# Optimization experiments

Measured on AMD Instinct MI355X. Metric: run time of the kernel, lower is better.

## Reference

```python
import jax, jax.numpy as jnp
import numpy as np

H = 50  # hidden_layer_size

def lstm_layer(x_seq, W_ih, W_hh, b_ih, b_hh):
    """x_seq: [B,T,D]. Returns hidden sequence [T,B,H]. PyTorch gate order i,f,g,o."""
    B = x_seq.shape[0]
    # Precompute input contribution for all timesteps in one GEMM: [B,T,4H]
    xW = jnp.einsum('btd,gd->btg', x_seq, W_ih) + b_ih + b_hh
    xW = jnp.transpose(xW, (1, 0, 2))  # [T,B,4H] for scan over time
    h0 = jnp.zeros((B, H), dtype=x_seq.dtype)
    c0 = jnp.zeros((B, H), dtype=x_seq.dtype)

    def step(carry, xt):
        h, c = carry
        gates = xt + h @ W_hh.T  # [B,4H]
        i, f, g, o = jnp.split(gates, 4, axis=-1)
        i = jax.nn.sigmoid(i)
        f = jax.nn.sigmoid(f)
        g = jnp.tanh(g)
        o = jax.nn.sigmoid(o)
        c = f * c + i * g
        h = o * jnp.tanh(c)
        return (h, c), h

    (_, _), hs = jax.lax.scan(step, (h0, c0), xW)
    return hs  # [T,B,H]


def setup_inputs() -> dict:
    key = jax.random.key(0)
    ks = jax.random.split(key, 12)
    B, T, D = 4096, 512, 5
    s_in = 1.0 / np.sqrt(H)

    def u(k, shape):
        return jax.random.uniform(k, shape, jnp.float32, -s_in, s_in)

    return {
        'input_seq': jax.random.normal(ks[0], (B, T, D), jnp.float32),
        'W_ih_l0': u(ks[1], (4 * H, D)),
        'W_hh_l0': u(ks[2], (4 * H, H)),
        'b_ih_l0': u(ks[3], (4 * H,)),
        'b_hh_l0': u(ks[4], (4 * H,)),
        'W_ih_l1': u(ks[5], (4 * H, H)),
        'W_hh_l1': u(ks[6], (4 * H, H)),
        'b_ih_l1': u(ks[7], (4 * H,)),
        'b_hh_l1': u(ks[8], (4 * H,)),
        'W_lin': u(ks[9], (1, H)),
        'b_lin': u(ks[10], (1,)),
    }


def reference(input_seq, W_ih_l0, W_hh_l0, b_ih_l0, b_hh_l0,
              W_ih_l1, W_hh_l1, b_ih_l1, b_hh_l1, W_lin, b_lin):
    hs0 = lstm_layer(input_seq, W_ih_l0, W_hh_l0, b_ih_l0, b_hh_l0)       # [T,B,H]
    hs1 = lstm_layer(jnp.transpose(hs0, (1, 0, 2)), W_ih_l1, W_hh_l1, b_ih_l1, b_hh_l1)
    last = hs1[-1]                       # [B,H] == out[:, -1, :]
    return last @ W_lin.T + b_lin        # [B,1]
```

## Files before the change

kernel.cpp:

```cpp
#include <hip/hip_runtime.h>

#define TSTEPS 512
#define NB     16
#define NW     13
#define WGS    (NW * 64)

typedef _Float16 f16x8 __attribute__((ext_vector_type(8)));
typedef float    f32x4 __attribute__((ext_vector_type(4)));

#define NKF  4
#define PARF 2048


__global__ __launch_bounds__(WGS)
void lstm_mfma5(const float* __restrict__ x,
                const float* __restrict__ Wih0, const float* __restrict__ Whh0,
                const float* __restrict__ bih0, const float* __restrict__ bhh0,
                const float* __restrict__ Wih1, const float* __restrict__ Whh1,
                const float* __restrict__ bih1, const float* __restrict__ bhh1,
                const float* __restrict__ Wlin, const float* __restrict__ blin,
                float* __restrict__ out)
{
    __shared__ __align__(16) _Float16 Bbuf[2][NKF][64][8];
    __shared__ float h1f[NB][52];

    const int tid    = threadIdx.x;
    const int w      = tid >> 6;
    const int l      = tid & 63;
    const int sg     = l >> 4;
    const int bcol   = l & 15;
    const int batch0 = blockIdx.x * NB;

    _Float16* bbase = &Bbuf[0][0][0][0];

    {
        int* bz = (int*)bbase;
        for (int i = tid; i < 2048; i += WGS) bz[i] = 0;
    }
    __syncthreads();

    auto baddr = [&](int k, int col) -> int {
        int kf = k >> 5, kl = k & 31;
        return (kf * 64 + col + (((kl >> 2) & 3) << 4)) * 8
               + ((kl & 3) | (((kl >> 4) & 1) << 2));
    };

    const bool xact = (tid < NB * 5);
    const int  xb = tid / 5, xd = tid % 5;
    const float* xptr = x + (size_t)(batch0 + xb) * TSTEPS * 5 + xd;
    int xadr = 0;
    if (xact) {
        xadr = baddr(50 + xd, xb);
        bbase[PARF + xadr] = (_Float16)xptr[0];
        bbase[xadr]        = (_Float16)xptr[5];
    }

    f16x8 A0[2], A1[NKF];
    f32x4 bia0, bia1;
    float c0 = 0.f, c1 = 0.f;
    {
        const int arow = w * 16 + bcol;
        const int jj   = arow >> 2;
        const int gt   = arow & 3;
        const bool real = (jj < 50);
        const int row  = gt * 50 + jj;
        const float s  = (gt == 2) ? 2.885390082f : -1.442695041f;
        #pragma unroll
        for (int kf = 0; kf < 2; ++kf) {
            f16x8 a;
            #pragma unroll
            for (int e = 0; e < 8; ++e) {
                int k = kf * 32 + 4 * sg + (e & 3) + ((e >> 2) << 4);
                float v = 0.f;
                if (real) {
                    if (k < 50)      v = Whh0[row * 50 + k];
                    else if (k < 55) v = Wih0[row * 5 + (k - 50)];
                }
                a[e] = (_Float16)(s * v);
            }
            A0[kf] = a;
        }
        #pragma unroll
        for (int kf = 0; kf < NKF; ++kf) {
            f16x8 a;
            #pragma unroll
            for (int e = 0; e < 8; ++e) {
                int k = kf * 32 + 4 * sg + (e & 3) + ((e >> 2) << 4);
                float v = 0.f;
                if (real) {
                    if (k < 50)                  v = Wih1[row * 50 + k];
                    else if (k >= 56 && k < 106) v = Whh1[row * 50 + (k - 56)];
                }
                a[e] = (_Float16)(s * v);
            }
            A1[kf] = a;
        }
    }
    const int j   = 4 * w + sg;
    const bool jok = (j < 50);
    {
        f32x4 b0, b1;
        #pragma unroll
        for (int r = 0; r < 4; ++r) {
            const float sr = (r == 2) ? 2.885390082f : -1.442695041f;
            b0[r] = jok ? sr * (bih0[r * 50 + j] + bhh0[r * 50 + j]) : 0.f;
            b1[r] = jok ? sr * (bih1[r * 50 + j] + bhh1[r * 50 + j]) : 0.f;
        }
        bia0 = b0; bia1 = b1;
    }

    const int adrH0 = jok ? baddr(j, bcol) : 0;
    const int adrH1 = jok ? baddr(56 + j, bcol) : 0;

    auto update = [&](const f32x4& acc, float& c, int wadr) -> float {
        float iv = __builtin_amdgcn_rcpf(1.0f + __builtin_amdgcn_exp2f(acc[0]));
        float fv = __builtin_amdgcn_rcpf(1.0f + __builtin_amdgcn_exp2f(acc[1]));
        float gv = 1.0f - 2.0f * __builtin_amdgcn_rcpf(1.0f + __builtin_amdgcn_exp2f(acc[2]));
        float ov = __builtin_amdgcn_rcpf(1.0f + __builtin_amdgcn_exp2f(acc[3]));
        c = fv * c + iv * gv;
        float th = 1.0f - 2.0f * __builtin_amdgcn_rcpf(1.0f + __builtin_amdgcn_exp2f(2.885390082f * c));
        float h = ov * th;
        if (jok) bbase[wadr] = (_Float16)h;
        return h;
    };

    const _Float16* vbase = &Bbuf[0][0][l][0];
    __syncthreads();

    {
        const _Float16* rd = vbase + PARF;
        f32x4 a = bia0;
        a = __builtin_amdgcn_mfma_f32_16x16x32_f16(A0[0], *(const f16x8*)(rd), a, 0, 0, 0);
        a = __builtin_amdgcn_mfma_f32_16x16x32_f16(A0[1], *(const f16x8*)(rd + 512), a, 0, 0, 0);
        update(a, c0, adrH0);
    }
    float xv_next = xact ? xptr[10] : 0.f;
    __syncthreads();

#define REGION(PAR, T)                                                           \
    {                                                                            \
        const _Float16* rd = vbase + (PAR) * PARF;                               \
        const int wo = ((PAR) ^ 1) * PARF;                                       \
        f16x8 bf0 = *(const f16x8*)(rd);                                         \
        f16x8 bf1 = *(const f16x8*)(rd + 512);                                   \
        f16x8 bf2 = *(const f16x8*)(rd + 1024);                                  \
        f16x8 bf3 = *(const f16x8*)(rd + 1536);                                  \
        if (xact && (T) + 2 < TSTEPS) bbase[wo + xadr] = (_Float16)xv_next;      \
        float xv2 = (xact && (T) + 3 < TSTEPS) ? xptr[((T) + 3) * 5] : 0.f;      \
        f32x4 aB = bia1;                                                         \
        aB = __builtin_amdgcn_mfma_f32_16x16x32_f16(A1[0], bf0, aB, 0, 0, 0);    \
        aB = __builtin_amdgcn_mfma_f32_16x16x32_f16(A1[1], bf1, aB, 0, 0, 0);    \
        aB = __builtin_amdgcn_mfma_f32_16x16x32_f16(A1[2], bf2, aB, 0, 0, 0);    \
        aB = __builtin_amdgcn_mfma_f32_16x16x32_f16(A1[3], bf3, aB, 0, 0, 0);    \
        f32x4 aA = bia0;                                                         \
        aA = __builtin_amdgcn_mfma_f32_16x16x32_f16(A0[0], bf0, aA, 0, 0, 0);    \
        aA = __builtin_amdgcn_mfma_f32_16x16x32_f16(A0[1], bf1, aA, 0, 0, 0);    \
        float h1v = update(aB, c1, wo + adrH1);                                  \
        update(aA, c0, wo + adrH0);                                              \
        if ((T) == TSTEPS - 1 && jok) h1f[bcol][j] = h1v;                        \
        xv_next = xv2;                                                           \
        __syncthreads();                                                         \
    }

    for (int t = 0; t < TSTEPS; t += 2) {
        REGION(0, t)
        REGION(1, t + 1)
    }
#undef REGION

    if (tid < NB) {
        float acc = blin[0];
        #pragma unroll 10
        for (int jj = 0; jj < 50; ++jj) acc += Wlin[jj] * h1f[tid][jj];
        out[batch0 + tid] = acc;
    }
}

extern "C" void kernel_launch(void* const* d_in, const int* in_sizes, int n_in,
                              void* d_out, int out_size, void* d_ws, size_t ws_size,
                              hipStream_t stream) {
    (void)in_sizes; (void)n_in; (void)d_ws; (void)ws_size; (void)out_size;
    const float* x    = (const float*)d_in[0];
    const float* Wih0 = (const float*)d_in[1];
    const float* Whh0 = (const float*)d_in[2];
    const float* bih0 = (const float*)d_in[3];
    const float* bhh0 = (const float*)d_in[4];
    const float* Wih1 = (const float*)d_in[5];
    const float* Whh1 = (const float*)d_in[6];
    const float* bih1 = (const float*)d_in[7];
    const float* bhh1 = (const float*)d_in[8];
    const float* Wlin = (const float*)d_in[9];
    const float* blin = (const float*)d_in[10];
    float* out = (float*)d_out;

    dim3 grid(4096 / NB);
    dim3 block(WGS);
    hipLaunchKernelGGL(lstm_mfma5, grid, block, 0, stream,
                       x, Wih0, Whh0, bih0, bhh0,
                       Wih1, Whh1, bih1, bhh1, Wlin, blin, out);
}
```

Baseline: 354.3 us.

## Fold biases into MFMA via constant-one row, split layer-1 accumulation chain

Places a constant 1.0 in the unused K slot 55 of the shared B operand and stores the combined biases in the matching A-matrix column, so every MFMA chain starts from zero instead of from a bias register. The layer-1 four-MFMA dependent chain is split into two independent two-MFMA chains that are summed afterwards, shortening the serial latency on the recurrent critical path. The per-step __syncthreads is replaced by an explicit lgkmcnt wait, s_barrier and sched_barrier to control scheduling. The trade-offs are an extra vector add per step and the bias now being rounded to fp16.

```diff
diff --git a/kernel.cpp b/kernel.cpp
--- a/kernel.cpp
+++ b/kernel.cpp
@@ -13,7 +13,7 @@
 
 
 __global__ __launch_bounds__(WGS)
-void lstm_mfma5(const float* __restrict__ x,
+void lstm_mfma6(const float* __restrict__ x,
                 const float* __restrict__ Wih0, const float* __restrict__ Whh0,
                 const float* __restrict__ bih0, const float* __restrict__ bhh0,
                 const float* __restrict__ Wih1, const float* __restrict__ Whh1,
@@ -45,6 +45,10 @@
                + ((kl & 3) | (((kl >> 4) & 1) << 2));
     };
 
+    if (tid < 32) {
+        int par = tid >> 4, col = tid & 15;
+        bbase[par * PARF + baddr(55, col)] = (_Float16)1.0f;
+    }
     const bool xact = (tid < NB * 5);
     const int  xb = tid / 5, xd = tid % 5;
     const float* xptr = x + (size_t)(batch0 + xb) * TSTEPS * 5 + xd;
@@ -56,7 +60,6 @@
     }
 
     f16x8 A0[2], A1[NKF];
-    f32x4 bia0, bia1;
     float c0 = 0.f, c1 = 0.f;
     {
         const int arow = w * 16 + bcol;
@@ -73,8 +76,9 @@
                 int k = kf * 32 + 4 * sg + (e & 3) + ((e >> 2) << 4);
                 float v = 0.f;
                 if (real) {
-                    if (k < 50)      v = Whh0[row * 50 + k];
-                    else if (k < 55) v = Wih0[row * 5 + (k - 50)];
+                    if (k < 50)       v = Whh0[row * 50 + k];
+                    else if (k < 55)  v = Wih0[row * 5 + (k - 50)];
+                    else if (k == 55) v = bih0[row] + bhh0[row];
                 }
                 a[e] = (_Float16)(s * v);
             }
@@ -89,6 +93,7 @@
                 float v = 0.f;
                 if (real) {
                     if (k < 50)                  v = Wih1[row * 50 + k];
+                    else if (k == 55)            v = bih1[row] + bhh1[row];
                     else if (k >= 56 && k < 106) v = Whh1[row * 50 + (k - 56)];
                 }
                 a[e] = (_Float16)(s * v);
@@ -98,16 +103,6 @@
     }
     const int j   = 4 * w + sg;
     const bool jok = (j < 50);
-    {
-        f32x4 b0, b1;
-        #pragma unroll
-        for (int r = 0; r < 4; ++r) {
-            const float sr = (r == 2) ? 2.885390082f : -1.442695041f;
-            b0[r] = jok ? sr * (bih0[r * 50 + j] + bhh0[r * 50 + j]) : 0.f;
-            b1[r] = jok ? sr * (bih1[r * 50 + j] + bhh1[r * 50 + j]) : 0.f;
-        }
-        bia0 = b0; bia1 = b1;
-    }
 
     const int adrH0 = jok ? baddr(j, bcol) : 0;
     const int adrH1 = jok ? baddr(56 + j, bcol) : 0;
@@ -125,41 +120,43 @@
     };
 
     const _Float16* vbase = &Bbuf[0][0][l][0];
+    const f32x4 Z = {0.f, 0.f, 0.f, 0.f};
     __syncthreads();
 
     {
         const _Float16* rd = vbase + PARF;
-        f32x4 a = bia0;
-        a = __builtin_amdgcn_mfma_f32_16x16x32_f16(A0[0], *(const f16x8*)(rd), a, 0, 0, 0);
+        f32x4 a;
+        a = __builtin_amdgcn_mfma_f32_16x16x32_f16(A0[0], *(const f16x8*)(rd), Z, 0, 0, 0);
         a = __builtin_amdgcn_mfma_f32_16x16x32_f16(A0[1], *(const f16x8*)(rd + 512), a, 0, 0, 0);
         update(a, c0, adrH0);
     }
     float xv_next = xact ? xptr[10] : 0.f;
     __syncthreads();
 
-#define REGION(PAR, T)                                                           \
-    {                                                                            \
-        const _Float16* rd = vbase + (PAR) * PARF;                               \
-        const int wo = ((PAR) ^ 1) * PARF;                                       \
-        f16x8 bf0 = *(const f16x8*)(rd);                                         \
-        f16x8 bf1 = *(const f16x8*)(rd + 512);                                   \
-        f16x8 bf2 = *(const f16x8*)(rd + 1024);                                  \
-        f16x8 bf3 = *(const f16x8*)(rd + 1536);                                  \
-        if (xact && (T) + 2 < TSTEPS) bbase[wo + xadr] = (_Float16)xv_next;      \
-        float xv2 = (xact && (T) + 3 < TSTEPS) ? xptr[((T) + 3) * 5] : 0.f;      \
-        f32x4 aB = bia1;                                                         \
-        aB = __builtin_amdgcn_mfma_f32_16x16x32_f16(A1[0], bf0, aB, 0, 0, 0);    \
-        aB = __builtin_amdgcn_mfma_f32_16x16x32_f16(A1[1], bf1, aB, 0, 0, 0);    \
-        aB = __builtin_amdgcn_mfma_f32_16x16x32_f16(A1[2], bf2, aB, 0, 0, 0);    \
-        aB = __builtin_amdgcn_mfma_f32_16x16x32_f16(A1[3], bf3, aB, 0, 0, 0);    \
-        f32x4 aA = bia0;                                                         \
-        aA = __builtin_amdgcn_mfma_f32_16x16x32_f16(A0[0], bf0, aA, 0, 0, 0);    \
-        aA = __builtin_amdgcn_mfma_f32_16x16x32_f16(A0[1], bf1, aA, 0, 0, 0);    \
-        float h1v = update(aB, c1, wo + adrH1);                                  \
-        update(aA, c0, wo + adrH0);                                              \
-        if ((T) == TSTEPS - 1 && jok) h1f[bcol][j] = h1v;                        \
-        xv_next = xv2;                                                           \
-        __syncthreads();                                                         \
+#define REGION(PAR, T)                                                             \
+    {                                                                              \
+        const _Float16* rd = vbase + (PAR) * PARF;                                 \
+        const int wo = ((PAR) ^ 1) * PARF;                                         \
+        f16x8 bf0 = *(const f16x8*)(rd);                                           \
+        f16x8 bf1 = *(const f16x8*)(rd + 512);                                     \
+        f16x8 bf2 = *(const f16x8*)(rd + 1024);                                    \
+        f16x8 bf3 = *(const f16x8*)(rd + 1536);                                    \
+        if (xact && (T) + 2 < TSTEPS) bbase[wo + xadr] = (_Float16)xv_next;        \
+        float xv2 = (xact && (T) + 3 < TSTEPS) ? xptr[((T) + 3) * 5] : 0.f;        \
+        f32x4 aB1 = __builtin_amdgcn_mfma_f32_16x16x32_f16(A1[0], bf0, Z, 0, 0, 0);\
+        aB1 = __builtin_amdgcn_mfma_f32_16x16x32_f16(A1[1], bf1, aB1, 0, 0, 0);    \
+        f32x4 aB2 = __builtin_amdgcn_mfma_f32_16x16x32_f16(A1[2], bf2, Z, 0, 0, 0);\
+        aB2 = __builtin_amdgcn_mfma_f32_16x16x32_f16(A1[3], bf3, aB2, 0, 0, 0);    \
+        f32x4 aA = __builtin_amdgcn_mfma_f32_16x16x32_f16(A0[0], bf0, Z, 0, 0, 0); \
+        aA = __builtin_amdgcn_mfma_f32_16x16x32_f16(A0[1], bf1, aA, 0, 0, 0);      \
+        f32x4 aB = aB1 + aB2;                                                      \
+        float h1v = update(aB, c1, wo + adrH1);                                    \
+        update(aA, c0, wo + adrH0);                                                \
+        if ((T) == TSTEPS - 1 && jok) h1f[bcol][j] = h1v;                          \
+        xv_next = xv2;                                                             \
+        asm volatile("s_waitcnt lgkmcnt(0)" ::: "memory");                         \
+        __builtin_amdgcn_s_barrier();                                              \
+        __builtin_amdgcn_sched_barrier(0);                                         \
     }
 
     for (int t = 0; t < TSTEPS; t += 2) {
@@ -167,6 +164,8 @@
         REGION(1, t + 1)
     }
 #undef REGION
+
+    __syncthreads();
 
     if (tid < NB) {
         float acc = blin[0];
@@ -195,7 +194,7 @@
 
     dim3 grid(4096 / NB);
     dim3 block(WGS);
-    hipLaunchKernelGGL(lstm_mfma5, grid, block, 0, stream,
+    hipLaunchKernelGGL(lstm_mfma6, grid, block, 0, stream,
                        x, Wih0, Whh0, bih0, bhh0,
                        Wih1, Whh1, bih1, bhh1, Wlin, blin, out);
 }
```

After: 388.5 us. +9.6%, slower.
